# Kernel optimization log

Measured on AMD Instinct MI355X. Metric: run time of the kernel, lower is better.

Reference implementation:

```python
import jax, jax.numpy as jnp
import numpy as np

EPS = 1e-06


def setup_inputs() -> dict:
    key = jax.random.key(0)
    ks = jax.random.split(key, 8)
    B, N, D, r, T, O, Hid = 32, 2048, 64, 32, 31, 12, 128
    in_dim = r + T  # 63
    xav = lambda k, shape: jax.random.uniform(k, shape, jnp.float32, -1.0, 1.0) * np.sqrt(6.0 / (shape[0] + shape[1]))
    return {
        "H": jax.random.normal(ks[0], (B, N, D), jnp.float32),
        "ts_out": jax.random.uniform(ks[1], (B, O, T), jnp.float32),
        "O": O,
        "P_raw": xav(ks[2], (N, r)),
        "Q_raw": xav(ks[3], (N, r)),
        "W1": xav(ks[4], (in_dim, Hid)),
        "b1": jnp.zeros((Hid,), jnp.float32),
        "W2": xav(ks[5], (Hid, r)),
        "b2": jnp.zeros((r,), jnp.float32),
        "alpha": jax.random.uniform(ks[6], (1,), jnp.float32),
    }


def reference(H, ts_out, O, P_raw, Q_raw, W1, b1, W2, b2, alpha):
    # nonnegative_basis=True -> softplus on both bases
    P = jax.nn.softplus(P_raw)  # [N, r]
    Q = jax.nn.softplus(Q_raw)  # [N, r]
    # Right contraction: U = Q^T H per batch -> [B, r, D]
    U = jnp.einsum('bnd,nr->brd', H, Q)
    # Context norm over feature dim: [B, r]
    ctx = jnp.sqrt(jnp.mean(U * U, axis=-1) + EPS)
    # Gate features: concat([ts_out [B,O,T], ctx broadcast to [B,O,r]])
    B = H.shape[0]
    ctx_exp = jnp.broadcast_to(ctx[:, None, :], (B, O, ctx.shape[-1]))
    feat = jnp.concatenate([ts_out, ctx_exp], axis=-1)  # [B, O, T+r]
    # scale MLP with exact (erf) GELU, dropout=0 (eval)
    h = jax.nn.gelu(feat @ W1 + b1, approximate=False)
    s = jax.nn.softplus(h @ W2 + b2)  # [B, O, r]
    # M = P (s \odot U) without materializing NxN: [B, O, N, D]
    M = jnp.einsum('bor,brd,nr->bond', s, U, P)
    a = jnp.clip(alpha[0], 0.0, 1.0)
    H_base = H[:, None, :, :]  # broadcast over O
    H_graph = H_base + a * (M - H_base)
    return H_graph
```

## Files before the change

kernel.cpp:

```cpp
#include <hip/hip_runtime.h>
#include <math.h>

#define B_ 32
#define N_ 2048
#define D_ 64
#define R_ 32
#define T_ 31
#define O_ 12
#define HID_ 128
#define IN_DIM_ 63
#define NCH_ 32

#define OFF_QSP   0
#define OFF_UPART (OFF_QSP + N_*R_)
#define OFF_U     (OFF_UPART + B_*NCH_*R_*D_)
#define OFF_CTX   (OFF_U + B_*R_*D_)
#define OFF_PBF   (OFF_CTX + B_*R_)
#define OFF_SUT   (OFF_PBF + N_*R_/2)

typedef __attribute__((ext_vector_type(4))) float f32x4;
typedef __attribute__((ext_vector_type(8))) short short8;

__device__ __forceinline__ float softplus_f(float x) {
    return fmaxf(x, 0.0f) + log1pf(expf(-fabsf(x)));
}
__device__ __forceinline__ float gelu_f(float x) {
    return 0.5f * x * (1.0f + erff(x * 0.70710678118654752440f));
}
__device__ __forceinline__ unsigned short f2bf(float f) {
    unsigned int u = __float_as_uint(f);
    u = (u + 0x7FFFu + ((u >> 16) & 1u)) >> 16;
    return (unsigned short)u;
}

__global__ __launch_bounds__(256) void k_softplus(const float* __restrict__ Qr,
                                                  const float* __restrict__ Pr,
                                                  float* __restrict__ ws) {
    int i = blockIdx.x * blockDim.x + threadIdx.x;
    if (i < N_ * R_) {
        ws[OFF_QSP + i] = softplus_f(Qr[i]);
    } else if (i < 2 * N_ * R_) {
        int j = i - N_ * R_;
        ((unsigned short*)(ws + OFF_PBF))[j] = f2bf(softplus_f(Pr[j]));
    }
}

__global__ __launch_bounds__(512) void k_upart(const float* __restrict__ H,
                                               float* __restrict__ ws) {
    const float* __restrict__ Qsp = ws + OFF_QSP;
    float* __restrict__ Upart = ws + OFF_UPART;
    int b = blockIdx.x / NCH_;
    int c = blockIdx.x % NCH_;
    int tid = threadIdx.x;
    int d = tid & 63;
    int rb = __builtin_amdgcn_readfirstlane(tid >> 6);
    const int r0 = rb * 4;
    float acc0 = 0.f, acc1 = 0.f, acc2 = 0.f, acc3 = 0.f;
    const int n0 = c * (N_ / NCH_);
    const float* __restrict__ Hb = H + (size_t)b * N_ * D_ + d;
    #pragma unroll 2
    for (int i = 0; i < N_ / NCH_; ++i) {
        int n = n0 + i;
        float h = Hb[(size_t)n * D_];
        const float* q = Qsp + (size_t)n * R_ + r0;
        acc0 = fmaf(h, q[0], acc0);
        acc1 = fmaf(h, q[1], acc1);
        acc2 = fmaf(h, q[2], acc2);
        acc3 = fmaf(h, q[3], acc3);
    }
    float* up = Upart + ((size_t)(b * NCH_ + c) * R_ + r0) * D_ + d;
    up[0 * D_] = acc0;
    up[1 * D_] = acc1;
    up[2 * D_] = acc2;
    up[3 * D_] = acc3;
}

__global__ __launch_bounds__(256) void k_ured(float* __restrict__ ws) {
    const float* __restrict__ Upart = ws + OFF_UPART;
    float* __restrict__ U = ws + OFF_U;
    float* __restrict__ ctx = ws + OFF_CTX;
    int b = blockIdx.x;
    int r = blockIdx.y * 4 + (threadIdx.x >> 6);
    int d = threadIdx.x & 63;
    float u = 0.f;
    #pragma unroll 8
    for (int c = 0; c < NCH_; ++c)
        u += Upart[((size_t)(b * NCH_ + c) * R_ + r) * D_ + d];
    U[((size_t)b * R_ + r) * D_ + d] = u;
    float sq = u * u;
    #pragma unroll
    for (int off = 32; off; off >>= 1) sq += __shfl_xor(sq, off, 64);
    if (d == 0) ctx[b * R_ + r] = sqrtf(sq * (1.0f / D_) + 1e-6f);
}

__global__ __launch_bounds__(128) void k_mlp(const float* __restrict__ ts_out,
                                             const float* __restrict__ W1,
                                             const float* __restrict__ b1,
                                             const float* __restrict__ W2,
                                             const float* __restrict__ b2,
                                             const float* __restrict__ alpha,
                                             float* __restrict__ ws) {
    __shared__ float feat[IN_DIM_];
    __shared__ float hsh[HID_];
    __shared__ float ssh[R_];
    int bo = blockIdx.x;
    int b = bo / O_;
    int tid = threadIdx.x;
    const float* __restrict__ ctx = ws + OFF_CTX;
    if (tid < T_) feat[tid] = ts_out[(size_t)bo * T_ + tid];
    else if (tid < IN_DIM_) feat[tid] = ctx[b * R_ + (tid - T_)];
    __syncthreads();
    float acc = b1[tid];
    #pragma unroll 9
    for (int k = 0; k < IN_DIM_; ++k) acc = fmaf(feat[k], W1[k * HID_ + tid], acc);
    hsh[tid] = gelu_f(acc);
    __syncthreads();
    if (tid < R_) {
        float a2 = b2[tid];
        #pragma unroll 8
        for (int j = 0; j < HID_; ++j) a2 = fmaf(hsh[j], W2[j * R_ + tid], a2);
        ssh[tid] = softplus_f(a2);
    }
    __syncthreads();
    float a = fminf(fmaxf(alpha[0], 0.0f), 1.0f);
    const float* __restrict__ U = ws + OFF_U;
    unsigned short* SUT = (unsigned short*)(ws + OFF_SUT) + (size_t)bo * D_ * R_;
    #pragma unroll
    for (int idx = tid; idx < D_ * R_; idx += 128) {
        int d = idx >> 5, r = idx & 31;
        SUT[idx] = f2bf(a * ssh[r] * U[((size_t)b * R_ + r) * D_ + d]);
    }
}

__global__ __launch_bounds__(256) void k_main(const float* __restrict__ H,
                                              const float* __restrict__ alpha,
                                              const float* __restrict__ ws,
                                              float* __restrict__ out) {
    __shared__ float tile[2 * 64 * 64];
    const int b = blockIdx.y;
    const int nblk = blockIdx.x * 64;
    const int tid = threadIdx.x;
    const int w = tid >> 6;
    const int lane = tid & 63;
    const int l16 = lane & 15;
    const int lhi = lane >> 4;
    const int rl = w * 16 + l16;
    const float a = fminf(fmaxf(alpha[0], 0.0f), 1.0f);
    const float oma = 1.0f - a;

    const unsigned short* Pbf = (const unsigned short*)(ws + OFF_PBF);
    const unsigned short* SUT0 = (const unsigned short*)(ws + OFF_SUT);

    short8 pfrag = *(const short8*)(Pbf + (size_t)(nblk + rl) * R_ + lhi * 8);

    const float* __restrict__ Hrow = H + ((size_t)b * N_ + nblk + rl) * D_;
    f32x4 homa[4];
    #pragma unroll
    for (int db = 0; db < 4; ++db)
        homa[db] = oma * *(const f32x4*)(Hrow + db * 16 + lhi * 4);

    char* t0 = (char*)tile;
    char* t1 = (char*)tile + 16384;
    float* __restrict__ oblk = out + ((size_t)(b * O_) * N_ + nblk) * D_;

    for (int o = 0; o < O_; o += 2) {
        const unsigned short* S0 = SUT0 + (size_t)(b * O_ + o) * D_ * R_;
        const unsigned short* S1 = S0 + D_ * R_;
        short8 sf[8];
        #pragma unroll
        for (int db = 0; db < 4; ++db) {
            sf[db]     = *(const short8*)(S0 + (size_t)(db * 16 + l16) * R_ + lhi * 8);
            sf[4 + db] = *(const short8*)(S1 + (size_t)(db * 16 + l16) * R_ + lhi * 8);
        }
        #pragma unroll
        for (int h = 0; h < 2; ++h) {
            char* tb = h ? t1 : t0;
            #pragma unroll
            for (int db = 0; db < 4; ++db) {
                f32x4 v = homa[db] + __builtin_amdgcn_mfma_f32_16x16x32_bf16(
                    sf[h * 4 + db], pfrag, (f32x4){0.f, 0.f, 0.f, 0.f}, 0, 0, 0);
                int c = (db * 64 + lhi * 16) ^ ((rl & 7) << 4);
                *(f32x4*)(tb + rl * 256 + c) = v;
            }
        }
        #pragma unroll
        for (int h = 0; h < 2; ++h) {
            char* tb = h ? t1 : t0;
            char* op = (char*)(oblk + (size_t)(o + h) * N_ * D_);
            #pragma unroll
            for (int i = 0; i < 4; ++i) {
                int g = w * 4096 + i * 1024 + lane * 16;
                int rr = g >> 8;
                int cc = (g & 255) ^ ((rr & 7) << 4);
                f32x4 v = *(const f32x4*)(tb + rr * 256 + cc);
                *(f32x4*)(op + g) = v;
            }
        }
    }
}

extern "C" void kernel_launch(void* const* d_in, const int* in_sizes, int n_in,
                              void* d_out, int out_size, void* d_ws, size_t ws_size,
                              hipStream_t stream) {
    const float* H      = (const float*)d_in[0];
    const float* ts_out = (const float*)d_in[1];
    const float* P_raw  = (const float*)d_in[3];
    const float* Q_raw  = (const float*)d_in[4];
    const float* W1     = (const float*)d_in[5];
    const float* b1     = (const float*)d_in[6];
    const float* W2     = (const float*)d_in[7];
    const float* b2     = (const float*)d_in[8];
    const float* alpha  = (const float*)d_in[9];
    float* out = (float*)d_out;
    float* ws  = (float*)d_ws;

    k_softplus<<<dim3((2 * N_ * R_ + 255) / 256), dim3(256), 0, stream>>>(Q_raw, P_raw, ws);
    k_upart<<<dim3(B_ * NCH_), dim3(512), 0, stream>>>(H, ws);
    k_ured<<<dim3(B_, 8), dim3(256), 0, stream>>>(ws);
    k_mlp<<<dim3(B_ * O_), dim3(128), 0, stream>>>(ts_out, W1, b1, W2, b2, alpha, ws);
    k_main<<<dim3(N_ / 64, B_), dim3(256), 0, stream>>>(H, alpha, ws, out);
}
```

Before: 73.68 us.

## Fuse softplus into U partial kernel and merge reduction, MLP, SUT per batch

Computes the Q softplus inside the U partial-sum kernel and broadcasts it with readlane, and writes the bf16 P softplus from the batch-0 blocks. The U reduction, context norm, gate MLP and scaled-U construction are merged into one kernel with one block per batch, keeping U and ctx in shared memory. This removes two kernel launches and workspace round trips. The trade-off is that the MLP stage now runs on only 32 blocks, which lowers parallelism there.

```diff
diff --git a/kernel.cpp b/kernel.cpp
--- a/kernel.cpp
+++ b/kernel.cpp
@@ -11,11 +11,8 @@
 #define IN_DIM_ 63
 #define NCH_ 32
 
-#define OFF_QSP   0
-#define OFF_UPART (OFF_QSP + N_*R_)
-#define OFF_U     (OFF_UPART + B_*NCH_*R_*D_)
-#define OFF_CTX   (OFF_U + B_*R_*D_)
-#define OFF_PBF   (OFF_CTX + B_*R_)
+#define OFF_UPART 0
+#define OFF_PBF   (OFF_UPART + B_*NCH_*R_*D_)
 #define OFF_SUT   (OFF_PBF + N_*R_/2)
 
 typedef __attribute__((ext_vector_type(4))) float f32x4;
@@ -33,102 +30,110 @@
     return (unsigned short)u;
 }
 
-__global__ __launch_bounds__(256) void k_softplus(const float* __restrict__ Qr,
-                                                  const float* __restrict__ Pr,
-                                                  float* __restrict__ ws) {
-    int i = blockIdx.x * blockDim.x + threadIdx.x;
-    if (i < N_ * R_) {
-        ws[OFF_QSP + i] = softplus_f(Qr[i]);
-    } else if (i < 2 * N_ * R_) {
-        int j = i - N_ * R_;
-        ((unsigned short*)(ws + OFF_PBF))[j] = f2bf(softplus_f(Pr[j]));
-    }
-}
-
-__global__ __launch_bounds__(512) void k_upart(const float* __restrict__ H,
+__global__ __launch_bounds__(512) void k_front(const float* __restrict__ H,
+                                               const float* __restrict__ Qr,
+                                               const float* __restrict__ Pr,
                                                float* __restrict__ ws) {
-    const float* __restrict__ Qsp = ws + OFF_QSP;
     float* __restrict__ Upart = ws + OFF_UPART;
     int b = blockIdx.x / NCH_;
     int c = blockIdx.x % NCH_;
     int tid = threadIdx.x;
-    int d = tid & 63;
-    int rb = __builtin_amdgcn_readfirstlane(tid >> 6);
-    const int r0 = rb * 4;
+    int lane = tid & 63;
+    int w = __builtin_amdgcn_readfirstlane(tid >> 6);
+    const int r0 = w * 4;
+    const int n0 = c * 64;
+
+    if (b == 0) {
+        unsigned short* Pbf = (unsigned short*)(ws + OFF_PBF);
+        for (int i = tid; i < 64 * R_; i += 512)
+            Pbf[(size_t)n0 * R_ + i] = f2bf(softplus_f(Pr[(size_t)n0 * R_ + i]));
+    }
+
+    const float* qrow = Qr + (size_t)(n0 + lane) * R_ + r0;
+    float q0 = softplus_f(qrow[0]);
+    float q1 = softplus_f(qrow[1]);
+    float q2 = softplus_f(qrow[2]);
+    float q3 = softplus_f(qrow[3]);
+
     float acc0 = 0.f, acc1 = 0.f, acc2 = 0.f, acc3 = 0.f;
-    const int n0 = c * (N_ / NCH_);
-    const float* __restrict__ Hb = H + (size_t)b * N_ * D_ + d;
-    #pragma unroll 2
-    for (int i = 0; i < N_ / NCH_; ++i) {
-        int n = n0 + i;
-        float h = Hb[(size_t)n * D_];
-        const float* q = Qsp + (size_t)n * R_ + r0;
-        acc0 = fmaf(h, q[0], acc0);
-        acc1 = fmaf(h, q[1], acc1);
-        acc2 = fmaf(h, q[2], acc2);
-        acc3 = fmaf(h, q[3], acc3);
-    }
-    float* up = Upart + ((size_t)(b * NCH_ + c) * R_ + r0) * D_ + d;
+    const float* __restrict__ Hb = H + ((size_t)b * N_ + n0) * D_ + lane;
+    #pragma unroll 4
+    for (int i = 0; i < 64; ++i) {
+        float h = Hb[(size_t)i * D_];
+        float s0 = __int_as_float(__builtin_amdgcn_readlane(__float_as_int(q0), i));
+        float s1 = __int_as_float(__builtin_amdgcn_readlane(__float_as_int(q1), i));
+        float s2 = __int_as_float(__builtin_amdgcn_readlane(__float_as_int(q2), i));
+        float s3 = __int_as_float(__builtin_amdgcn_readlane(__float_as_int(q3), i));
+        acc0 = fmaf(h, s0, acc0);
+        acc1 = fmaf(h, s1, acc1);
+        acc2 = fmaf(h, s2, acc2);
+        acc3 = fmaf(h, s3, acc3);
+    }
+    float* up = Upart + ((size_t)(b * NCH_ + c) * R_ + r0) * D_ + lane;
     up[0 * D_] = acc0;
     up[1 * D_] = acc1;
     up[2 * D_] = acc2;
     up[3 * D_] = acc3;
 }
 
-__global__ __launch_bounds__(256) void k_ured(float* __restrict__ ws) {
+__global__ __launch_bounds__(512) void k_tail(const float* __restrict__ ts_out,
+                                              const float* __restrict__ W1,
+                                              const float* __restrict__ b1,
+                                              const float* __restrict__ W2,
+                                              const float* __restrict__ b2,
+                                              const float* __restrict__ alpha,
+                                              float* __restrict__ ws) {
+    __shared__ float Ul[R_][D_];
+    __shared__ float ctxl[R_];
+    __shared__ float tsl[O_ * T_];
+    __shared__ float hsh[O_][HID_];
+    __shared__ float ssh[O_][R_];
+    int b = blockIdx.x;
+    int tid = threadIdx.x;
     const float* __restrict__ Upart = ws + OFF_UPART;
-    float* __restrict__ U = ws + OFF_U;
-    float* __restrict__ ctx = ws + OFF_CTX;
-    int b = blockIdx.x;
-    int r = blockIdx.y * 4 + (threadIdx.x >> 6);
-    int d = threadIdx.x & 63;
-    float u = 0.f;
-    #pragma unroll 8
-    for (int c = 0; c < NCH_; ++c)
-        u += Upart[((size_t)(b * NCH_ + c) * R_ + r) * D_ + d];
-    U[((size_t)b * R_ + r) * D_ + d] = u;
-    float sq = u * u;
+
+    {
+        int r = tid >> 4;
+        int d0 = (tid & 15) * 4;
+        f32x4 u = {0.f, 0.f, 0.f, 0.f};
+        #pragma unroll 8
+        for (int c = 0; c < NCH_; ++c)
+            u += *(const f32x4*)(Upart + ((size_t)(b * NCH_ + c) * R_ + r) * D_ + d0);
+        *(f32x4*)(&Ul[r][d0]) = u;
+        float sq = u[0]*u[0] + u[1]*u[1] + u[2]*u[2] + u[3]*u[3];
+        #pragma unroll
+        for (int off = 8; off; off >>= 1) sq += __shfl_xor(sq, off, 16);
+        if ((tid & 15) == 0) ctxl[r] = sqrtf(sq * (1.0f / D_) + 1e-6f);
+    }
+    for (int i = tid; i < O_ * T_; i += 512)
+        tsl[i] = ts_out[(size_t)b * O_ * T_ + i];
+    __syncthreads();
+
+    int g = tid >> 7;
+    int lt = tid & 127;
     #pragma unroll
-    for (int off = 32; off; off >>= 1) sq += __shfl_xor(sq, off, 64);
-    if (d == 0) ctx[b * R_ + r] = sqrtf(sq * (1.0f / D_) + 1e-6f);
-}
-
-__global__ __launch_bounds__(128) void k_mlp(const float* __restrict__ ts_out,
-                                             const float* __restrict__ W1,
-                                             const float* __restrict__ b1,
-                                             const float* __restrict__ W2,
-                                             const float* __restrict__ b2,
-                                             const float* __restrict__ alpha,
-                                             float* __restrict__ ws) {
-    __shared__ float feat[IN_DIM_];
-    __shared__ float hsh[HID_];
-    __shared__ float ssh[R_];
-    int bo = blockIdx.x;
-    int b = bo / O_;
-    int tid = threadIdx.x;
-    const float* __restrict__ ctx = ws + OFF_CTX;
-    if (tid < T_) feat[tid] = ts_out[(size_t)bo * T_ + tid];
-    else if (tid < IN_DIM_) feat[tid] = ctx[b * R_ + (tid - T_)];
+    for (int oo = 0; oo < 3; ++oo) {
+        int o = g + oo * 4;
+        float acc = b1[lt];
+        for (int k = 0; k < T_; ++k) acc = fmaf(tsl[o * T_ + k], W1[k * HID_ + lt], acc);
+        for (int k = 0; k < R_; ++k) acc = fmaf(ctxl[k], W1[(T_ + k) * HID_ + lt], acc);
+        hsh[o][lt] = gelu_f(acc);
+    }
     __syncthreads();
-    float acc = b1[tid];
-    #pragma unroll 9
-    for (int k = 0; k < IN_DIM_; ++k) acc = fmaf(feat[k], W1[k * HID_ + tid], acc);
-    hsh[tid] = gelu_f(acc);
+    if (tid < O_ * R_) {
+        int o = tid >> 5, r = tid & 31;
+        float a2 = b2[r];
+        #pragma unroll 8
+        for (int j = 0; j < HID_; ++j) a2 = fmaf(hsh[o][j], W2[j * R_ + r], a2);
+        ssh[o][r] = softplus_f(a2);
+    }
     __syncthreads();
-    if (tid < R_) {
-        float a2 = b2[tid];
-        #pragma unroll 8
-        for (int j = 0; j < HID_; ++j) a2 = fmaf(hsh[j], W2[j * R_ + tid], a2);
-        ssh[tid] = softplus_f(a2);
-    }
-    __syncthreads();
+
     float a = fminf(fmaxf(alpha[0], 0.0f), 1.0f);
-    const float* __restrict__ U = ws + OFF_U;
-    unsigned short* SUT = (unsigned short*)(ws + OFF_SUT) + (size_t)bo * D_ * R_;
-    #pragma unroll
-    for (int idx = tid; idx < D_ * R_; idx += 128) {
-        int d = idx >> 5, r = idx & 31;
-        SUT[idx] = f2bf(a * ssh[r] * U[((size_t)b * R_ + r) * D_ + d]);
+    unsigned short* SUT = (unsigned short*)(ws + OFF_SUT) + (size_t)b * O_ * D_ * R_;
+    for (int idx = tid; idx < O_ * D_ * R_; idx += 512) {
+        int r = idx & 31, d = (idx >> 5) & 63, o = idx >> 11;
+        SUT[idx] = f2bf(a * ssh[o][r] * Ul[r][d]);
     }
 }
 
@@ -189,11 +194,11 @@
             char* op = (char*)(oblk + (size_t)(o + h) * N_ * D_);
             #pragma unroll
             for (int i = 0; i < 4; ++i) {
-                int g = w * 4096 + i * 1024 + lane * 16;
-                int rr = g >> 8;
-                int cc = (g & 255) ^ ((rr & 7) << 4);
+                int gg = w * 4096 + i * 1024 + lane * 16;
+                int rr = gg >> 8;
+                int cc = (gg & 255) ^ ((rr & 7) << 4);
                 f32x4 v = *(const f32x4*)(tb + rr * 256 + cc);
-                *(f32x4*)(op + g) = v;
+                *(f32x4*)(op + gg) = v;
             }
         }
     }
@@ -214,9 +219,7 @@
     float* out = (float*)d_out;
     float* ws  = (float*)d_ws;
 
-    k_softplus<<<dim3((2 * N_ * R_ + 255) / 256), dim3(256), 0, stream>>>(Q_raw, P_raw, ws);
-    k_upart<<<dim3(B_ * NCH_), dim3(512), 0, stream>>>(H, ws);
-    k_ured<<<dim3(B_, 8), dim3(256), 0, stream>>>(ws);
-    k_mlp<<<dim3(B_ * O_), dim3(128), 0, stream>>>(ts_out, W1, b1, W2, b2, alpha, ws);
+    k_front<<<dim3(B_ * NCH_), dim3(512), 0, stream>>>(H, Q_raw, P_raw, ws);
+    k_tail<<<dim3(B_), dim3(512), 0, stream>>>(ts_out, W1, b1, W2, b2, alpha, ws);
     k_main<<<dim3(N_ / 64, B_), dim3(256), 0, stream>>>(H, alpha, ws, out);
 }
```

Result: slower. 84.83 us (+15.1%).
